# Optimization experiments

Measured on AMD Instinct MI355X. Metric: run time of the kernel, lower is better.

## Reference

```python
import jax, jax.numpy as jnp
import numpy as np

# dims (match init_kwargs)
B, M, L, T = 32, 64, 512, 96
P, S, D = 8, 4, 64
KS = 4          # depthwise conv1d kernel (kernel_size)
K1 = 3          # conv2d_kernel (conv_ffn1 width kernel)
R = 2           # ffn expansion r
N = L // S      # 128 tokens per variable


def _same_pad(k):
    # torch Conv padding='same' (stride 1): left = (k-1)//2, right = (k-1) - left
    t = k - 1
    return (t // 2, t - t // 2)


def conv1d(x, w, b, stride=1, padding='VALID', groups=1):
    y = jax.lax.conv_general_dilated(x, w, (stride,), padding,
                                     dimension_numbers=('NCH', 'OIH', 'NCH'),
                                     feature_group_count=groups)
    return y + b[None, :, None]


def conv2d(x, w, b, padding):
    y = jax.lax.conv_general_dilated(x, w, (1, 1), padding,
                                     dimension_numbers=('NCHW', 'OIHW', 'NCHW'))
    return y + b[None, :, None, None]


def setup_inputs() -> dict:
    key = jax.random.key(0)
    ks = jax.random.split(key, 20)
    def rnd(k, shape, fan_in):
        return (jax.random.normal(k, shape, jnp.float32) / np.sqrt(fan_in)).astype(jnp.float32)
    inp = {
        'x': jax.random.normal(ks[0], (B, M, L), jnp.float32),
        'emb_w': rnd(ks[1], (D, 1, P), P),
        'emb_b': jnp.zeros((D,), jnp.float32),
        'head_w': rnd(ks[2], (T, D * N), D * N),
        'head_b': jnp.zeros((T,), jnp.float32),
    }
    for i, base in [(1, 3), (2, 10)]:
        inp[f'dw_w{i}'] = rnd(ks[base], (N * D, 1, KS), KS)
        inp[f'dw_b{i}'] = jnp.zeros((N * D,), jnp.float32)
        inp[f'f{i}1_w'] = rnd(ks[base + 1], (R * D, D, 4, K1), D * 4 * K1)
        inp[f'f{i}1_b'] = jnp.zeros((R * D,), jnp.float32)
        inp[f'f{i}2_w'] = rnd(ks[base + 2], (D, R * D, 4, K1), R * D * 4 * K1)
        inp[f'f{i}2_b'] = jnp.zeros((D,), jnp.float32)
    return inp


def _embed(x, emb_w, emb_b):
    # x: [B, M, L] -> [(B*M), 1, L] -> replicate-pad right by P-S -> conv1d stride S
    xr = x.reshape(B * M, 1, L)
    xp = jnp.pad(xr, ((0, 0), (0, 0), (0, P - S)), mode='edge')
    y = conv1d(xp, emb_w, emb_b, stride=S)          # [(B*M), D, N]
    return y.reshape(B, M, D, N)


def _block(x_emb, dw_w, dw_b, f1_w, f1_b, f2_w, f2_b):
    # x_emb: [B, M, D, N]
    x = x_emb.transpose(0, 3, 2, 1)                 # [B, N, D, M]
    x = x.reshape(B, N * D, M)
    x = conv1d(x, dw_w, dw_b, padding=[_same_pad(KS)], groups=N * D)  # depthwise over M
    x = x.reshape(B, N, D, M)
    x = x.transpose(0, 2, 3, 1)                     # [B, D, M, N]
    pad = [_same_pad(4), _same_pad(K1)]
    h = jax.nn.gelu(conv2d(x, f1_w, f1_b, pad), approximate=False)    # [B, R*D, M, N]
    x = conv2d(h, f2_w, f2_b, pad)                  # [B, D, M, N]
    x = x.transpose(0, 2, 1, 3)                     # [B, M, D, N]
    return x + x_emb


def reference(x, emb_w, emb_b, dw_w1, dw_b1, f11_w, f11_b, f12_w, f12_b,
              dw_w2, dw_b2, f21_w, f21_b, f22_w, f22_b, head_w, head_b):
    x_emb = _embed(x, emb_w, emb_b)
    x_emb = _block(x_emb, dw_w1, dw_b1, f11_w, f11_b, f12_w, f12_b)
    x_emb = _block(x_emb, dw_w2, dw_b2, f21_w, f21_b, f22_w, f22_b)
    z = x_emb.reshape(B, M, D * N)
    pred = jnp.einsum('bmf,tf->bmt', z, head_w) + head_b   # [B, M, T]
    return pred
```

## Files before the change

kernel.cpp:

```cpp
#include <hip/hip_runtime.h>
#include <hip/hip_bf16.h>
#include <math.h>

#define MMX 64
#define NNX 128
#define DDX 64
#define RDX 128
#define TTX 96
#define LLX 512
#define PROWS 67
#define PCOLS 130

typedef short bfx8 __attribute__((ext_vector_type(8)));
typedef float floatx4 __attribute__((ext_vector_type(4)));

__device__ __forceinline__ float gelu(float v) {
  return 0.5f * v * (1.0f + erff(v * 0.70710678118654752f));
}

__device__ __forceinline__ void gload_lds16(const void* g, void* l) {
  __builtin_amdgcn_global_load_lds(
      (const __attribute__((address_space(1))) unsigned int*)g,
      (__attribute__((address_space(3))) unsigned int*)l, 16, 0, 0);
}

__global__ __launch_bounds__(256) void castw_kernel(
    const float* __restrict__ w, __hip_bfloat16* __restrict__ o, int CO, int CI) {
  int i = blockIdx.x * 256 + threadIdx.x;
  int ci = i % CI;
  int t = i / CI;
  int co = t % CO;
  int dd = t / CO;
  o[i] = __float2bfloat16(w[(size_t)(co * CI + ci) * 12 + dd]);
}

__global__ __launch_bounds__(256) void headw_kernel(
    const float* __restrict__ hw, __hip_bfloat16* __restrict__ o) {
  int i = blockIdx.x * 256 + threadIdx.x;
  int fh = i & 8191;
  int t = i >> 13;
  int d = fh & 63;
  int n = fh >> 6;
  o[i] = __float2bfloat16(hw[(size_t)t * 8192 + d * 128 + n]);
}

__global__ __launch_bounds__(256) void embed_kernel(
    const float* __restrict__ x, const float* __restrict__ w,
    const float* __restrict__ bias, float* __restrict__ xe, int bm_off) {
  int tid = blockIdx.x * 256 + threadIdx.x;
  int d  = tid & 63;
  int n  = (tid >> 6) & 127;
  int bm = tid >> 13;
  const float* xr = x + (size_t)(bm_off + bm) * LLX;
  float acc = bias[d];
  int base = n * 4;
#pragma unroll
  for (int p = 0; p < 8; ++p) {
    int i = base + p;
    if (i > LLX - 1) i = LLX - 1;
    acc += w[d * 8 + p] * xr[i];
  }
  xe[tid] = acc;
}

__global__ __launch_bounds__(256) void dw_kernel(
    const float* __restrict__ xe, const float* __restrict__ w,
    const float* __restrict__ bias, __hip_bfloat16* __restrict__ yp) {
  const int tid = threadIdx.x;
  const int d = tid & 63;
  const int n = ((blockIdx.x & 31) << 2) + (tid >> 6);
  const int b = blockIdx.x >> 5;
  const int c = n * DDX + d;
  const float w0 = w[c * 4 + 0], w1 = w[c * 4 + 1];
  const float w2 = w[c * 4 + 2], w3 = w[c * 4 + 3];
  const float bv = bias[c];
  const float* src = xe + ((size_t)b * MMX * NNX + n) * DDX + d;
  __hip_bfloat16* dst = yp + (((size_t)b * PROWS + 1) * PCOLS + n + 1) * DDX + d;
  const int sstr = NNX * DDX;
  const int dstr = PCOLS * DDX;
  float xm1 = 0.f, x0 = src[0], xp1 = src[sstr], xp2;
#pragma unroll 4
  for (int m = 0; m < MMX; ++m) {
    xp2 = (m + 2 < MMX) ? src[(size_t)(m + 2) * sstr] : 0.f;
    float acc = bv + w0 * xm1 + w1 * x0 + w2 * xp1 + w3 * xp2;
    dst[(size_t)m * dstr] = __float2bfloat16(acc);
    xm1 = x0; x0 = xp1; xp1 = xp2;
  }
}

template <int CIN, int COUT, bool GELU, int WPX>
__global__ __launch_bounds__(256) void conv_lds(
    const __hip_bfloat16* __restrict__ in,
    const __hip_bfloat16* __restrict__ wT,
    const float* __restrict__ bias,
    __hip_bfloat16* __restrict__ hout,
    float* xio,
    __hip_bfloat16* __restrict__ xb) {
  constexpr int KC = CIN / 32;
  constexpr int WCO = 4 / WPX;
  constexpr int PT = 8 / WPX;
  constexpr int CT = COUT / 16 / WCO;
  constexpr int NS = CIN / 8;
  constexpr int TOTCH = 130 * NS;
  constexpr int PER = (TOTCH + 255) / 256;
  constexpr int EPI = GELU ? 64 * (COUT + 8) : 64 * (COUT + 4) * 2;
  constexpr int SMEMN = (130 * CIN > EPI) ? 130 * CIN : EPI;
  __shared__ short smem[SMEMN];

  const int nwg = gridDim.x;
  const int wid = (blockIdx.x & 7) * (nwg >> 3) + (blockIdx.x >> 3);
  const int m = wid & 63;
  const int b = wid >> 6;
  const int tid = threadIdx.x;
  const int lane = tid & 63;
  const int w = tid >> 6;
  const int wco = w % WCO;
  const int wpx = w / WCO;
  const int wc0 = wco * (16 * CT);
  const int px0 = wpx * (16 * PT);
  const int l15 = lane & 15;
  const int quad = lane >> 4;

  floatx4 acc[PT][CT];
#pragma unroll
  for (int i = 0; i < PT; ++i)
#pragma unroll
    for (int j = 0; j < CT; ++j) acc[i][j] = (floatx4)0.f;

  const __hip_bfloat16* inrow = in + ((size_t)b * PROWS + m) * PCOLS * CIN;

#pragma unroll 1
  for (int dm = 0; dm < 4; ++dm) {
    __syncthreads();
    {
      const __hip_bfloat16* rowp = inrow + (size_t)dm * PCOLS * CIN;
#pragma unroll
      for (int p = 0; p < PER; ++p) {
        int s = tid + p * 256;
        if (s < TOTCH) {
          int r = s / NS, c = s % NS;
          int cs = c ^ (r & (NS - 1));
          gload_lds16(rowp + (size_t)r * CIN + cs * 8, smem + s * 8);
        }
      }
    }
    __syncthreads();

    const __hip_bfloat16* wbase = wT + (size_t)dm * 3 * COUT * CIN;
#pragma unroll
    for (int dn = 0; dn < 3; ++dn) {
      bfx8 Bf[KC][CT];
#pragma unroll
      for (int kc = 0; kc < KC; ++kc)
#pragma unroll
        for (int j = 0; j < CT; ++j)
          Bf[kc][j] = *(const bfx8*)(
              wbase + ((size_t)dn * COUT + wc0 + 16 * j + l15) * CIN +
              kc * 32 + quad * 8);
#pragma unroll
      for (int kc = 0; kc < KC; ++kc) {
#pragma unroll
        for (int i = 0; i < PT; ++i) {
          const int rowa = px0 + 16 * i + l15 + dn;
          const int slot = kc * 4 + quad;
          bfx8 a = *(const bfx8*)&smem[rowa * CIN +
                                       ((slot ^ (rowa & (NS - 1))) << 3)];
#pragma unroll
          for (int j = 0; j < CT; ++j)
            acc[i][j] = __builtin_amdgcn_mfma_f32_16x16x32_bf16(
                a, Bf[kc][j], acc[i][j], 0, 0, 0);
        }
      }
    }
  }

  float bs[CT];
#pragma unroll
  for (int j = 0; j < CT; ++j) bs[j] = bias[wc0 + 16 * j + l15];

  __syncthreads();
#pragma unroll
  for (int h = 0; h < 2; ++h) {
    if (GELU) {
      constexpr int STR2 = COUT + 8;
      short* t2 = smem;
#pragma unroll
      for (int i = 0; i < PT; ++i) {
        int g = wpx * PT + i;
        if ((g >> 2) == h) {
          int ii = g & 3;
#pragma unroll
          for (int j = 0; j < CT; ++j)
#pragma unroll
            for (int r = 0; r < 4; ++r) {
              int pl = 16 * ii + quad * 4 + r;
              __hip_bfloat16 bv = __float2bfloat16(gelu(acc[i][j][r] + bs[j]));
              t2[pl * STR2 + wc0 + 16 * j + l15] = *(short*)&bv;
            }
        }
      }
      __syncthreads();
      constexpr int CHUNKS = 64 * COUT / 8;
      size_t gbase = (((size_t)b * PROWS + m + 1) * PCOLS + 1 + h * 64) * COUT;
      for (int idx = tid; idx < CHUNKS; idx += 256) {
        int px = idx / (COUT / 8), cg = idx % (COUT / 8);
        uint4 v = *(uint4*)&t2[px * STR2 + cg * 8];
        *(uint4*)(hout + gbase + (size_t)px * COUT + cg * 8) = v;
      }
      __syncthreads();
    } else {
      constexpr int STRF = COUT + 4;
      float* tf = (float*)smem;
#pragma unroll
      for (int i = 0; i < PT; ++i) {
        int g = wpx * PT + i;
        if ((g >> 2) == h) {
          int ii = g & 3;
#pragma unroll
          for (int j = 0; j < CT; ++j)
#pragma unroll
            for (int r = 0; r < 4; ++r) {
              int pl = 16 * ii + quad * 4 + r;
              tf[pl * STRF + wc0 + 16 * j + l15] = acc[i][j][r] + bs[j];
            }
        }
      }
      __syncthreads();
      constexpr int CHUNKS = 64 * COUT / 4;
      size_t gbase = (((size_t)b * MMX + m) * NNX + h * 64) * COUT;
      for (int idx = tid; idx < CHUNKS; idx += 256) {
        int px = idx / (COUT / 4), cg = idx % (COUT / 4);
        float4 a4 = *(float4*)&tf[px * STRF + cg * 4];
        size_t gx = gbase + (size_t)px * COUT + cg * 4;
        float4 xv = *(float4*)(xio + gx);
        float4 rr = make_float4(a4.x + xv.x, a4.y + xv.y, a4.z + xv.z, a4.w + xv.w);
        *(float4*)(xio + gx) = rr;
        __hip_bfloat16 o0 = __float2bfloat16(rr.x), o1 = __float2bfloat16(rr.y);
        __hip_bfloat16 o2 = __float2bfloat16(rr.z), o3 = __float2bfloat16(rr.w);
        ushort4 ov = make_ushort4(*(unsigned short*)&o0, *(unsigned short*)&o1,
                                  *(unsigned short*)&o2, *(unsigned short*)&o3);
        *(ushort4*)(xb + gx) = ov;
      }
      __syncthreads();
    }
  }
}

__global__ __launch_bounds__(256) void head_split(
    const __hip_bfloat16* __restrict__ xb,
    const __hip_bfloat16* __restrict__ hwT,
    float* __restrict__ P, int nbm) {
  const int ks = blockIdx.x & 7;
  const int bm0 = (blockIdx.x >> 3) * 64;
  const int lane = threadIdx.x & 63;
  const int w = threadIdx.x >> 6;
  const int l15 = lane & 15;
  const int quad = lane >> 4;
  const int bmw = bm0 + w * 16;

  floatx4 acc[6];
#pragma unroll
  for (int j = 0; j < 6; ++j) acc[j] = (floatx4)0.f;

  const int k0 = ks * 1024;
  const __hip_bfloat16* abase = xb + (size_t)(bmw + l15) * 8192 + k0;
  const __hip_bfloat16* bbase = hwT + (size_t)l15 * 8192 + k0;
#pragma unroll 4
  for (int kc = 0; kc < 32; ++kc) {
    const int kb = kc * 32 + quad * 8;
    bfx8 a = *(const bfx8*)(abase + kb);
#pragma unroll
    for (int j = 0; j < 6; ++j) {
      bfx8 bv = *(const bfx8*)(bbase + (size_t)(16 * j) * 8192 + kb);
      acc[j] = __builtin_amdgcn_mfma_f32_16x16x32_bf16(a, bv, acc[j], 0, 0, 0);
    }
  }
#pragma unroll
  for (int j = 0; j < 6; ++j) {
    int t = 16 * j + l15;
#pragma unroll
    for (int r = 0; r < 4; ++r) {
      int bm = bmw + quad * 4 + r;
      P[((size_t)ks * nbm + bm) * TTX + t] = acc[j][r];
    }
  }
}

__global__ __launch_bounds__(256) void head_reduce(
    const float* __restrict__ P, const float* __restrict__ hb,
    float* __restrict__ out, int nbm, int bm_off) {
  int i = blockIdx.x * 256 + threadIdx.x;
  int t = i % TTX;
  int bm = i / TTX;
  float s = hb[t];
#pragma unroll
  for (int ks = 0; ks < 8; ++ks) s += P[((size_t)ks * nbm + bm) * TTX + t];
  out[(size_t)(bm_off + bm) * TTX + t] = s;
}

extern "C" void kernel_launch(void* const* d_in, const int* in_sizes, int n_in,
                              void* d_out, int out_size, void* d_ws, size_t ws_size,
                              hipStream_t stream) {
  const float* x      = (const float*)d_in[0];
  const float* emb_w  = (const float*)d_in[1];
  const float* emb_b  = (const float*)d_in[2];
  const float* head_w = (const float*)d_in[3];
  const float* head_b = (const float*)d_in[4];
  const float* dw_w1  = (const float*)d_in[5];
  const float* dw_b1  = (const float*)d_in[6];
  const float* f11_w  = (const float*)d_in[7];
  const float* f11_b  = (const float*)d_in[8];
  const float* f12_w  = (const float*)d_in[9];
  const float* f12_b  = (const float*)d_in[10];
  const float* dw_w2  = (const float*)d_in[11];
  const float* dw_b2  = (const float*)d_in[12];
  const float* f21_w  = (const float*)d_in[13];
  const float* f21_b  = (const float*)d_in[14];
  const float* f22_w  = (const float*)d_in[15];
  const float* f22_b  = (const float*)d_in[16];

  const size_t WEL = 98304, HWEL = 786432;
  __hip_bfloat16* wt11 = (__hip_bfloat16*)d_ws;
  __hip_bfloat16* wt12 = wt11 + WEL;
  __hip_bfloat16* wt21 = wt12 + WEL;
  __hip_bfloat16* wt22 = wt21 + WEL;
  __hip_bfloat16* hwT  = wt22 + WEL;
  char* dyn = (char*)(hwT + HWEL);
  const size_t fixed_bytes = (4 * WEL + HWEL) * 2;

  const size_t YP_B = (size_t)PROWS * PCOLS * DDX * 2;
  const size_t HP_B = (size_t)PROWS * PCOLS * RDX * 2;
  const size_t X_B  = (size_t)MMX * NNX * DDX * 4;
  const size_t XB_B = (size_t)MMX * NNX * DDX * 2;
  const size_t P_B  = (size_t)8 * MMX * TTX * 4;
  const size_t PER_B = YP_B + HP_B + X_B + XB_B + P_B;
  int Bc = 32;
  while (Bc > 1 && fixed_bytes + (size_t)Bc * PER_B > ws_size) Bc >>= 1;

  __hip_bfloat16* Yp = (__hip_bfloat16*)dyn;
  __hip_bfloat16* Hp = (__hip_bfloat16*)(dyn + (size_t)Bc * YP_B);
  float* X  = (float*)(dyn + (size_t)Bc * (YP_B + HP_B));
  __hip_bfloat16* Xb = (__hip_bfloat16*)(dyn + (size_t)Bc * (YP_B + HP_B + X_B));
  float* P  = (float*)(dyn + (size_t)Bc * (YP_B + HP_B + X_B + XB_B));
  const int nbm = Bc * MMX;

  castw_kernel<<<384, 256, 0, stream>>>(f11_w, wt11, RDX, DDX);
  castw_kernel<<<384, 256, 0, stream>>>(f12_w, wt12, DDX, RDX);
  castw_kernel<<<384, 256, 0, stream>>>(f21_w, wt21, RDX, DDX);
  castw_kernel<<<384, 256, 0, stream>>>(f22_w, wt22, DDX, RDX);
  headw_kernel<<<3072, 256, 0, stream>>>(head_w, hwT);
  hipMemsetAsync(Yp, 0, (size_t)Bc * (YP_B + HP_B), stream);

  for (int b0 = 0; b0 < 32; b0 += Bc) {
    int bm_off = b0 * MMX;
    embed_kernel<<<Bc * 2048, 256, 0, stream>>>(x, emb_w, emb_b, X, bm_off);

    for (int l = 0; l < 2; ++l) {
      const float* dwW = l ? dw_w2 : dw_w1;
      const float* dwB = l ? dw_b2 : dw_b1;
      const __hip_bfloat16* w1 = l ? wt21 : wt11;
      const float* b1 = l ? f21_b : f11_b;
      const __hip_bfloat16* w2 = l ? wt22 : wt12;
      const float* b2 = l ? f22_b : f12_b;

      dw_kernel<<<Bc * 32, 256, 0, stream>>>(X, dwW, dwB, Yp);
      conv_lds<DDX, RDX, true, 1>
          <<<Bc * MMX, 256, 0, stream>>>(Yp, w1, b1, Hp, nullptr, nullptr);
      conv_lds<RDX, DDX, false, 2>
          <<<Bc * MMX, 256, 0, stream>>>(Hp, w2, b2, nullptr, X, Xb);
    }

    head_split<<<Bc * 8, 256, 0, stream>>>(Xb, hwT, P, nbm);
    head_reduce<<<Bc * 24, 256, 0, stream>>>(P, head_b, (float*)d_out, nbm, bm_off);
  }
}
```

Baseline: 629.8 us.

## Double-buffer LDS input rows in GELU conv and prefetch weights before barrier

Adds a double-buffer template option to the LDS conv kernel, enabled only for the first (GELU) conv. That kernel now prefetches the next input row into the alternate LDS buffer while running MFMAs on the current one, which should hide global-to-LDS load latency. Both variants also load the first weight fragment before the staging barrier, so that register load overlaps the LDS fill. The cost is twice the LDS footprint for the first conv, which may lower occupancy.

```diff
diff --git a/kernel.cpp b/kernel.cpp
--- a/kernel.cpp
+++ b/kernel.cpp
@@ -88,7 +88,7 @@
   }
 }
 
-template <int CIN, int COUT, bool GELU, int WPX>
+template <int CIN, int COUT, bool GELU, int WPX, bool DB>
 __global__ __launch_bounds__(256) void conv_lds(
     const __hip_bfloat16* __restrict__ in,
     const __hip_bfloat16* __restrict__ wT,
@@ -101,10 +101,12 @@
   constexpr int PT = 8 / WPX;
   constexpr int CT = COUT / 16 / WCO;
   constexpr int NS = CIN / 8;
+  constexpr int ROW = 130 * CIN;
   constexpr int TOTCH = 130 * NS;
   constexpr int PER = (TOTCH + 255) / 256;
+  constexpr int NBUF = DB ? 2 : 1;
   constexpr int EPI = GELU ? 64 * (COUT + 8) : 64 * (COUT + 4) * 2;
-  constexpr int SMEMN = (130 * CIN > EPI) ? 130 * CIN : EPI;
+  constexpr int SMEMN = (NBUF * ROW > EPI) ? NBUF * ROW : EPI;
   __shared__ short smem[SMEMN];
 
   const int nwg = gridDim.x;
@@ -129,42 +131,66 @@
 
   const __hip_bfloat16* inrow = in + ((size_t)b * PROWS + m) * PCOLS * CIN;
 
+  auto stage = [&](int rdm, short* dst) {
+    const __hip_bfloat16* rowp = inrow + (size_t)rdm * PCOLS * CIN;
+#pragma unroll
+    for (int p = 0; p < PER; ++p) {
+      int s = tid + p * 256;
+      if (s < TOTCH) {
+        int r = s / NS, c = s % NS;
+        int cs = c ^ (r & (NS - 1));
+        gload_lds16(rowp + (size_t)r * CIN + cs * 8, dst + s * 8);
+      }
+    }
+  };
+
+  if (DB) {
+    stage(0, smem);
+    __syncthreads();
+  }
+
 #pragma unroll 1
   for (int dm = 0; dm < 4; ++dm) {
-    __syncthreads();
-    {
-      const __hip_bfloat16* rowp = inrow + (size_t)dm * PCOLS * CIN;
-#pragma unroll
-      for (int p = 0; p < PER; ++p) {
-        int s = tid + p * 256;
-        if (s < TOTCH) {
-          int r = s / NS, c = s % NS;
-          int cs = c ^ (r & (NS - 1));
-          gload_lds16(rowp + (size_t)r * CIN + cs * 8, smem + s * 8);
-        }
-      }
-    }
-    __syncthreads();
+    short* buf = DB ? (smem + (dm & 1) * ROW) : smem;
+    if (!DB) {
+      __syncthreads();
+      stage(dm, buf);
+    }
 
     const __hip_bfloat16* wbase = wT + (size_t)dm * 3 * COUT * CIN;
+    bfx8 Bf[KC][CT];
+#pragma unroll
+    for (int kc = 0; kc < KC; ++kc)
+#pragma unroll
+      for (int j = 0; j < CT; ++j)
+        Bf[kc][j] = *(const bfx8*)(
+            wbase + ((size_t)wc0 + 16 * j + l15) * CIN + kc * 32 + quad * 8);
+
+    if (DB) {
+      if (dm < 3) stage(dm + 1, smem + ((dm + 1) & 1) * ROW);
+    } else {
+      __syncthreads();
+    }
+
 #pragma unroll
     for (int dn = 0; dn < 3; ++dn) {
-      bfx8 Bf[KC][CT];
-#pragma unroll
-      for (int kc = 0; kc < KC; ++kc)
-#pragma unroll
-        for (int j = 0; j < CT; ++j)
-          Bf[kc][j] = *(const bfx8*)(
-              wbase + ((size_t)dn * COUT + wc0 + 16 * j + l15) * CIN +
-              kc * 32 + quad * 8);
+      if (dn) {
+#pragma unroll
+        for (int kc = 0; kc < KC; ++kc)
+#pragma unroll
+          for (int j = 0; j < CT; ++j)
+            Bf[kc][j] = *(const bfx8*)(
+                wbase + ((size_t)dn * COUT + wc0 + 16 * j + l15) * CIN +
+                kc * 32 + quad * 8);
+      }
 #pragma unroll
       for (int kc = 0; kc < KC; ++kc) {
 #pragma unroll
         for (int i = 0; i < PT; ++i) {
           const int rowa = px0 + 16 * i + l15 + dn;
           const int slot = kc * 4 + quad;
-          bfx8 a = *(const bfx8*)&smem[rowa * CIN +
-                                       ((slot ^ (rowa & (NS - 1))) << 3)];
+          bfx8 a = *(const bfx8*)&buf[rowa * CIN +
+                                      ((slot ^ (rowa & (NS - 1))) << 3)];
 #pragma unroll
           for (int j = 0; j < CT; ++j)
             acc[i][j] = __builtin_amdgcn_mfma_f32_16x16x32_bf16(
@@ -172,13 +198,14 @@
         }
       }
     }
-  }
+    if (DB) __syncthreads();
+  }
+  if (!DB) __syncthreads();
 
   float bs[CT];
 #pragma unroll
   for (int j = 0; j < CT; ++j) bs[j] = bias[wc0 + 16 * j + l15];
 
-  __syncthreads();
 #pragma unroll
   for (int h = 0; h < 2; ++h) {
     if (GELU) {
@@ -364,9 +391,9 @@
       const float* b2 = l ? f22_b : f12_b;
 
       dw_kernel<<<Bc * 32, 256, 0, stream>>>(X, dwW, dwB, Yp);
-      conv_lds<DDX, RDX, true, 1>
+      conv_lds<DDX, RDX, true, 1, true>
           <<<Bc * MMX, 256, 0, stream>>>(Yp, w1, b1, Hp, nullptr, nullptr);
-      conv_lds<RDX, DDX, false, 2>
+      conv_lds<RDX, DDX, false, 2, false>
           <<<Bc * MMX, 256, 0, stream>>>(Hp, w2, b2, nullptr, X, Xb);
     }
 
```

Measured after the change: 637.2 us. About the same (+1.2%).
